# Kernel optimization log

Hardware: AMD Instinct MI355X
Metric: run time of the kernel (lower is better)

Reference implementation:

```python
import jax, jax.numpy as jnp
import numpy as np

H = 501
T = 200
V = 71


def gru_layer(x, h0, W_ih, W_hh, b_ih, b_hh):
    # x: [B,T,I], h0: [B,H]; PyTorch GRU gate order: r, z, n
    gi = jnp.einsum('bti,gi->btg', x, W_ih) + b_ih  # [B,T,3H]

    def step(h, gi_t):
        gh = h @ W_hh.T + b_hh  # [B,3H]
        r = jax.nn.sigmoid(gi_t[:, :H] + gh[:, :H])
        z = jax.nn.sigmoid(gi_t[:, H:2 * H] + gh[:, H:2 * H])
        n = jnp.tanh(gi_t[:, 2 * H:] + r * gh[:, 2 * H:])
        h_new = (1.0 - z) * n + z * h
        return h_new, h_new

    h_last, ys = jax.lax.scan(step, h0, jnp.swapaxes(gi, 0, 1))
    return jnp.swapaxes(ys, 0, 1), h_last  # [B,T,H], [B,H]


def setup_inputs() -> dict:
    key = jax.random.key(0)
    ks = jax.random.split(key, 16)
    s = 1.0 / np.sqrt(H)
    u = lambda k, shp: jax.random.uniform(k, shp, jnp.float32, -s, s)
    return {
        'x': jax.random.normal(ks[0], (256, 1), jnp.float32),
        'W_ih1': u(ks[1], (3 * H, 1)), 'W_hh1': u(ks[2], (3 * H, H)),
        'b_ih1': u(ks[3], (3 * H,)), 'b_hh1': u(ks[4], (3 * H,)),
        'W_ih2': u(ks[5], (3 * H, H)), 'W_hh2': u(ks[6], (3 * H, H)),
        'b_ih2': u(ks[7], (3 * H,)), 'b_hh2': u(ks[8], (3 * H,)),
        'W_ih3': u(ks[9], (3 * H, H)), 'W_hh3': u(ks[10], (3 * H, H)),
        'b_ih3': u(ks[11], (3 * H,)), 'b_hh3': u(ks[12], (3 * H,)),
        'Wd': u(ks[13], (V, H)), 'bd': u(ks[14], (V,)),
    }


def reference(x, W_ih1, W_hh1, b_ih1, b_hh1, W_ih2, W_hh2, b_ih2, b_hh2,
              W_ih3, W_hh3, b_ih3, b_hh3, Wd, bd):
    B = x.shape[0]
    # repeat_vector: tile latent scalar across T timesteps -> [B,T,1]
    xr = jnp.broadcast_to(x[:, None, :], (B, T, 1))
    h0 = jnp.zeros((B, H), x.dtype)
    o1, h1 = gru_layer(xr, h0, W_ih1, W_hh1, b_ih1, b_hh1)
    o1 = jnp.tanh(o1)
    o2, h2 = gru_layer(o1, h1, W_ih2, W_hh2, b_ih2, b_hh2)
    o2 = jnp.tanh(o2)
    o3, _ = gru_layer(o2, h2, W_ih3, W_hh3, b_ih3, b_hh3)
    o3 = jnp.tanh(o3)
    logits = jax.nn.relu(jnp.einsum('bth,vh->btv', o3, Wd) + bd)  # [B,T,V]
    return logits
```

## Files before the change

### kernel.cpp

```cpp
#include <hip/hip_runtime.h>
#include <hip/hip_fp16.h>

typedef _Float16 half8 __attribute__((ext_vector_type(8)));
typedef float floatx16 __attribute__((ext_vector_type(16)));

#define HID 501
#define TT  200
#define BB  256
#define VV  71
#define HP  512

#define OFF_BAR   0ull
#define OFF_HFRAG 4096ull
#define SZ_HFRAG  (2ull*8*32*512*2)
#define OFF_HFIN  (OFF_HFRAG + SZ_HFRAG)
#define SZ_HFIN   (256ull*512*4)
#define OFF_GI1   (OFF_HFIN + SZ_HFIN)
#define SZ_GI1    (256ull*1536*4)
#define OFF_BIAS  (OFF_GI1 + SZ_GI1)
#define SZ_BIAS   (65536ull)
#define OFF_WD    (OFF_BIAS + SZ_BIAS)
#define SZ_WD     (96ull*512*2)
#define OFF_BD    (OFF_WD + SZ_WD)
#define SZ_BD     4096ull
#define OFF_W     (OFF_BD + SZ_BD)
#define SZ_W      (3ull*2*32*2*32*1024*2)
#define OFF_OFRAG (OFF_W + SZ_W)
#define SZ_OBUF   (8ull*200*32*512*2)
#define WS_NEED   (OFF_OFRAG + 2ull*SZ_OBUF)

#define COH_LD16(dst, p) \
  asm volatile("global_load_dwordx4 %0, %1, off sc0 sc1" : "=&v"(dst) : "v"(p) : "memory")
__device__ __forceinline__ void coh_store16(_Float16* p, half8 v) {
  asm volatile("global_store_dwordx4 %0, %1, off sc0 sc1" :: "v"(p), "v"(v) : "memory");
}
__device__ __forceinline__ void coh_st4(unsigned* p, unsigned v) {
  asm volatile("global_store_dword %0, %1, off sc0 sc1" :: "v"(p), "v"(v) : "memory");
}
__device__ __forceinline__ float tanh_fast(float x) {
  float e = __expf(2.f*x);
  return 1.f - 2.f/(e + 1.f);
}

__global__ __launch_bounds__(256) void prep_weights(
    const float* __restrict__ wih1, const float* __restrict__ whh1,
    const float* __restrict__ wih2, const float* __restrict__ whh2,
    const float* __restrict__ wih3, const float* __restrict__ whh3,
    _Float16* __restrict__ wbuf)
{
  const float* WIH[3] = {wih1, wih2, wih3};
  const float* WHH[3] = {whh1, whh2, whh3};
  const long total = 3ll << 21;
  for (long idx = (long)blockIdx.x*256 + threadIdx.x; idx < total; idx += (long)gridDim.x*256) {
    int k   = (int)(idx & 1023);
    int row = (int)((idx >> 10) & 31);
    int rt  = (int)((idx >> 15) & 1);
    int blk = (int)((idx >> 16) & 31);
    int L   = (int)(idx >> 21);
    int g, hl; bool ok;
    if (rt == 0) { g = row >> 4; hl = row & 15; ok = true; }
    else         { g = 2;        hl = row & 15; ok = (row < 16); }
    int hcol = blk*16 + hl;
    ok = ok && (hcol < HID);
    float w = 0.f;
    if (ok) {
      if (k < HP) { if (L > 0 && k < HID) w = WIH[L][(g*HID + hcol)*HID + k]; }
      else        { int kk = k - HP; if (kk < HID) w = WHH[L][(g*HID + hcol)*HID + kk]; }
    }
    _Float16 wh = (_Float16)w;
    _Float16 wl = (_Float16)(w - (float)wh);
    long oh = ((((long)(L*2+0)*32 + blk)*2 + rt)*32 + row)*1024 + k;
    long ol = ((((long)(L*2+1)*32 + blk)*2 + rt)*32 + row)*1024 + k;
    wbuf[oh] = wh;
    wbuf[ol] = wl;
  }
}

__global__ __launch_bounds__(256) void prep_misc(
    const float* __restrict__ x, const float* __restrict__ wih1,
    const float* __restrict__ bih1, const float* __restrict__ bhh1,
    const float* __restrict__ bih2, const float* __restrict__ bhh2,
    const float* __restrict__ bih3, const float* __restrict__ bhh3,
    const float* __restrict__ wd, const float* __restrict__ bd,
    float* __restrict__ gi1, float* __restrict__ bias,
    _Float16* __restrict__ wdbuf, float* __restrict__ bdbuf)
{
  const int N1 = 256*1536;
  const int N2 = 3*2*1536;
  const int N3 = 96*512;
  const int N4 = 96;
  for (int idx = blockIdx.x*256 + threadIdx.x; idx < N1+N2+N3+N4; idx += gridDim.x*256) {
    if (idx < N1) {
      int b = idx / 1536, m = idx % 1536;
      int g = m >> 9, hc = m & 511;
      float v = 0.f;
      if (hc < HID) { int r = g*HID + hc; v = x[b]*wih1[r] + bih1[r]; }
      gi1[idx] = v;
    } else if (idx < N1+N2) {
      int i2 = idx - N1;
      int L = i2 / (2*1536);
      int rest = i2 % (2*1536);
      int pl = rest / 1536, m = rest % 1536;
      int g = m >> 9, hc = m & 511;
      float v = 0.f;
      if (hc < HID) {
        int r = g*HID + hc;
        if (pl == 0) v = (L==0) ? 0.f : (L==1 ? bih2[r] : bih3[r]);
        else         v = (L==0) ? bhh1[r] : (L==1 ? bhh2[r] : bhh3[r]);
      }
      bias[i2] = v;
    } else if (idx < N1+N2+N3) {
      int i3 = idx - (N1+N2);
      int v = i3 >> 9, k = i3 & 511;
      float val = (v < VV && k < HID) ? wd[v*HID + k] : 0.f;
      wdbuf[i3] = (_Float16)val;
    } else {
      int v = idx - (N1+N2+N3);
      bdbuf[v] = (v < VV) ? bd[v] : 0.f;
    }
  }
}

template<int L>
__global__ __launch_bounds__(512, 1) void gru_layer_k(
    const _Float16* __restrict__ wbuf,
    const _Float16* __restrict__ osrc,
    _Float16* __restrict__ odst,
    _Float16* __restrict__ hfrag,
    float* __restrict__ hfin,
    const float* __restrict__ gi1,
    const float* __restrict__ bias,
    unsigned* __restrict__ flags)
{
  constexpr int KPW = (L==0) ? 4 : 8;
  const int bid  = blockIdx.x;
  const int tile = bid & 7;
  const int sl   = bid >> 3;
  const int tid  = threadIdx.x;
  const int w    = tid >> 6;
  const int lane = tid & 63;

  __shared__ float    ldsC[8][2][32][32];
  __shared__ _Float16 ldsH[2][32][16];

  half8 Wf[2][2][KPW];
  {
    int row = lane & 31;
    int kc  = (lane >> 5) << 3;
    int ks0 = (L==0) ? (32 + w*4) : (w*8);
    #pragma unroll
    for (int pl = 0; pl < 2; ++pl)
      #pragma unroll
      for (int rt = 0; rt < 2; ++rt)
        #pragma unroll
        for (int i = 0; i < KPW; ++i) {
          long off = ((((long)(L*2+pl)*32 + sl)*2 + rt)*32 + row)*1024 + (long)(ks0+i)*16 + kc;
          Wf[pl][rt][i] = *(const half8*)(wbuf + off);
        }
  }

  const int b     = tid & 31;
  const int hl    = (tid >> 5) & 15;
  const int bglob = tile*32 + b;
  const int hglob = sl*16 + hl;
  float hreg = 0.f;
  float bih[3], bhh[3], gi[3] = {0,0,0};
  if (L > 0) hreg = hfin[bglob*HP + hglob];
  #pragma unroll
  for (int g = 0; g < 3; ++g) {
    bih[g] = bias[(L*2+0)*1536 + g*512 + hglob];
    bhh[g] = bias[(L*2+1)*1536 + g*512 + hglob];
    if (L == 0) gi[g] = gi1[(long)bglob*1536 + g*512 + hglob];
  }

  const long hf_par  = 8ll*32*512;
  const long hf_tile = (long)tile*(32*512);
  const long ob_t    = (long)tile*200*(32*512);
  const long region  = (long)sl*512;
  unsigned* fl = flags + tile*32;
  unsigned dead = 0;

  half8 X[8];
  if (L > 0 && w < 4) {
    const _Float16* xb = osrc + ob_t + (long)(w*8)*512 + lane*8;
    #pragma unroll
    for (int i = 0; i < 8; ++i) X[i] = *(const half8*)(xb + i*512);
  }

  for (int t = 0; t < TT; ++t) {
    if (L > 0 && w < 4) {
      floatx16 C0, C1;
      #pragma unroll
      for (int i = 0; i < 16; ++i) { C0[i] = 0.f; C1[i] = 0.f; }
      #pragma unroll
      for (int i = 0; i < 8; ++i) {
        C0 = __builtin_amdgcn_mfma_f32_32x32x16_f16(Wf[0][0][i], X[i], C0, 0, 0, 0);
        C0 = __builtin_amdgcn_mfma_f32_32x32x16_f16(Wf[1][0][i], X[i], C0, 0, 0, 0);
        C1 = __builtin_amdgcn_mfma_f32_32x32x16_f16(Wf[0][1][i], X[i], C1, 0, 0, 0);
        C1 = __builtin_amdgcn_mfma_f32_32x32x16_f16(Wf[1][1][i], X[i], C1, 0, 0, 0);
      }
      {
        int tn = (t + 1 < TT) ? t + 1 : 0;
        const _Float16* xb = osrc + ob_t + (long)tn*(32*512) + (long)(w*8)*512 + lane*8;
        #pragma unroll
        for (int i = 0; i < 8; ++i) X[i] = *(const half8*)(xb + i*512);
      }
      int col = lane & 31, rb = (lane >> 5) << 2;
      #pragma unroll
      for (int r = 0; r < 16; ++r) {
        int rowm = (r & 3) + 8*(r >> 2) + rb;
        ldsC[w][0][rowm][col] = C0[r];
        ldsC[w][1][rowm][col] = C1[r];
      }
    }
    if (t > 0) __syncthreads();
    if ((L == 0 || w >= 4) && !(L == 0 && t == 0)) {
      const int hs0 = (L==0) ? (w*4) : ((w-4)*8);
      const _Float16* hp = hfrag + (long)(t & 1)*hf_par + hf_tile + (long)hs0*512 + lane*8;
      half8 H[KPW];
      #pragma unroll
      for (int i = 0; i < KPW; ++i) COH_LD16(H[i], hp + i*512);
      asm volatile("s_waitcnt vmcnt(0)" ::: "memory");
      __builtin_amdgcn_sched_barrier(0);
      floatx16 C0, C1;
      #pragma unroll
      for (int i = 0; i < 16; ++i) { C0[i] = 0.f; C1[i] = 0.f; }
      #pragma unroll
      for (int i = 0; i < KPW; ++i) {
        C0 = __builtin_amdgcn_mfma_f32_32x32x16_f16(Wf[0][0][i], H[i], C0, 0, 0, 0);
        C0 = __builtin_amdgcn_mfma_f32_32x32x16_f16(Wf[1][0][i], H[i], C0, 0, 0, 0);
        C1 = __builtin_amdgcn_mfma_f32_32x32x16_f16(Wf[0][1][i], H[i], C1, 0, 0, 0);
        C1 = __builtin_amdgcn_mfma_f32_32x32x16_f16(Wf[1][1][i], H[i], C1, 0, 0, 0);
      }
      int col = lane & 31, rb = (lane >> 5) << 2;
      #pragma unroll
      for (int r = 0; r < 16; ++r) {
        int rowm = (r & 3) + 8*(r >> 2) + rb;
        ldsC[w][0][rowm][col] = C0[r];
        ldsC[w][1][rowm][col] = C1[r];
      }
    }
    __syncthreads();
    {
      float sx[3] = {0,0,0}, sh[3] = {0,0,0};
      if (!(L == 0 && t == 0)) {
        #pragma unroll
        for (int g = 0; g < 3; ++g) {
          int rt  = (g == 2) ? 1 : 0;
          int row = (g == 2) ? hl : g*16 + hl;
          float ax = 0.f, ah = 0.f;
          if (L == 0) {
            #pragma unroll
            for (int ww = 0; ww < 8; ++ww) ah += ldsC[ww][rt][row][b];
          } else {
            #pragma unroll
            for (int ww = 0; ww < 4; ++ww) ax += ldsC[ww][rt][row][b];
            #pragma unroll
            for (int ww = 4; ww < 8; ++ww) ah += ldsC[ww][rt][row][b];
          }
          sx[g] = ax; sh[g] = ah;
        }
      }
      float pr = sx[0] + gi[0] + bih[0] + sh[0] + bhh[0];
      float pz = sx[1] + gi[1] + bih[1] + sh[1] + bhh[1];
      float r = 1.f/(1.f + __expf(-pr));
      float z = 1.f/(1.f + __expf(-pz));
      float n = tanh_fast(sx[2] + gi[2] + bih[2] + r*(sh[2] + bhh[2]));
      float hn = (1.f - z)*n + z*hreg;
      hreg = hn;
      ldsH[0][b][hl] = (_Float16)hn;
      ldsH[1][b][hl] = (_Float16)tanh_fast(hn);
      if (t == TT-1) hfin[bglob*HP + hglob] = hn;
    }
    __syncthreads();
    if (tid < 64) {
      int h0 = (tid >> 5) * 8;
      half8 hv = *(const half8*)&ldsH[0][tid & 31][h0];
      coh_store16(hfrag + (long)((t+1) & 1)*hf_par + hf_tile + region + tid*8, hv);
    }
    if (w == 0) {
      asm volatile("s_waitcnt vmcnt(0)" ::: "memory");
      if (tid == 0 && t < TT-1)
        coh_st4(fl + sl, (unsigned)(L*(TT-1) + t + 1));
    }
    if (tid < 64) {
      int h0 = (tid >> 5) * 8;
      half8 ov = *(const half8*)&ldsH[1][tid & 31][h0];
      *(half8*)(odst + ob_t + (long)t*(32*512) + region + tid*8) = ov;
    }
    if (w == 5 && t < TT-1 && !dead) {
      const unsigned tgt = (unsigned)(L*(TT-1) + t + 1);
      const unsigned* fp = fl + (lane & 31);
      unsigned tries = 0;
      for (;;) {
        unsigned v0, v1, v2, v3;
        asm volatile(
          "global_load_dword %0, %4, off sc0 sc1\n\t"
          "global_load_dword %1, %4, off sc0 sc1\n\t"
          "global_load_dword %2, %4, off sc0 sc1\n\t"
          "global_load_dword %3, %4, off sc0 sc1"
          : "=&v"(v0), "=&v"(v1), "=&v"(v2), "=&v"(v3)
          : "v"(fp) : "memory");
        asm volatile("s_waitcnt vmcnt(3)" ::: "memory");
        __builtin_amdgcn_sched_barrier(0);
        if (__all(v0 >= tgt)) break;
        asm volatile("s_waitcnt vmcnt(2)" ::: "memory");
        __builtin_amdgcn_sched_barrier(0);
        if (__all(v1 >= tgt)) break;
        asm volatile("s_waitcnt vmcnt(1)" ::: "memory");
        __builtin_amdgcn_sched_barrier(0);
        if (__all(v2 >= tgt)) break;
        asm volatile("s_waitcnt vmcnt(0)" ::: "memory");
        __builtin_amdgcn_sched_barrier(0);
        if (__all(v3 >= tgt)) break;
        if (++tries > (1u<<17)) { dead = 1; break; }
      }
      asm volatile("s_waitcnt vmcnt(0)" ::: "memory");
    }
  }
}

__global__ __launch_bounds__(256, 2) void decoder_k(
    const _Float16* __restrict__ o3,
    const _Float16* __restrict__ wdbuf,
    const float* __restrict__ bdbuf,
    float* __restrict__ out)
{
  const int bx = blockIdx.x;
  const int tile = bx & 7;
  const int chunk = bx >> 3;
  const int tid = threadIdx.x;
  const int w = tid >> 6, lane = tid & 63;
  __shared__ float ldsD[4][96][32];
  __shared__ float ldsO[32][73];

  half8 Wf[3][8];
  {
    int kc = (lane >> 5) << 3;
    #pragma unroll
    for (int mt = 0; mt < 3; ++mt)
      #pragma unroll
      for (int i = 0; i < 8; ++i) {
        int row = mt*32 + (lane & 31);
        int k = (w*8 + i)*16 + kc;
        Wf[mt][i] = *(const half8*)(wdbuf + (long)row*512 + k);
      }
  }
  for (int tt = 0; tt < 8; ++tt) {
    int t = chunk*8 + tt;
    long ob = ((long)tile*200 + t)*(32*512);
    half8 Xf[8];
    #pragma unroll
    for (int i = 0; i < 8; ++i) {
      int s = w*8 + i;
      Xf[i] = *(const half8*)(o3 + ob + (long)s*512 + lane*8);
    }
    floatx16 C0, C1, C2;
    #pragma unroll
    for (int i = 0; i < 16; ++i) { C0[i] = 0.f; C1[i] = 0.f; C2[i] = 0.f; }
    #pragma unroll
    for (int i = 0; i < 8; ++i) {
      C0 = __builtin_amdgcn_mfma_f32_32x32x16_f16(Wf[0][i], Xf[i], C0, 0, 0, 0);
      C1 = __builtin_amdgcn_mfma_f32_32x32x16_f16(Wf[1][i], Xf[i], C1, 0, 0, 0);
      C2 = __builtin_amdgcn_mfma_f32_32x32x16_f16(Wf[2][i], Xf[i], C2, 0, 0, 0);
    }
    {
      int col = lane & 31;
      int rb = (lane >> 5) << 2;
      #pragma unroll
      for (int r = 0; r < 16; ++r) {
        int rowm = (r & 3) + 8*(r >> 2) + rb;
        ldsD[w][rowm][col]      = C0[r];
        ldsD[w][32 + rowm][col] = C1[r];
        ldsD[w][64 + rowm][col] = C2[r];
      }
    }
    __syncthreads();
    for (int ii = tid; ii < VV*32; ii += 256) {
      int bb = ii & 31, v = ii >> 5;
      float s = ldsD[0][v][bb] + ldsD[1][v][bb] + ldsD[2][v][bb] + ldsD[3][v][bb] + bdbuf[v];
      ldsO[bb][v] = s > 0.f ? s : 0.f;
    }
    __syncthreads();
    for (int ii = tid; ii < VV*32; ii += 256) {
      int bb = ii / VV, v = ii - bb*VV;
      out[((long)(tile*32 + bb)*200 + t)*VV + v] = ldsO[bb][v];
    }
    __syncthreads();
  }
}

extern "C" void kernel_launch(void* const* d_in, const int* in_sizes, int n_in,
                              void* d_out, int out_size, void* d_ws, size_t ws_size,
                              hipStream_t stream) {
  (void)in_sizes; (void)n_in;
  const float* x    = (const float*)d_in[0];
  const float* wih1 = (const float*)d_in[1];
  const float* whh1 = (const float*)d_in[2];
  const float* bih1 = (const float*)d_in[3];
  const float* bhh1 = (const float*)d_in[4];
  const float* wih2 = (const float*)d_in[5];
  const float* whh2 = (const float*)d_in[6];
  const float* bih2 = (const float*)d_in[7];
  const float* bhh2 = (const float*)d_in[8];
  const float* wih3 = (const float*)d_in[9];
  const float* whh3 = (const float*)d_in[10];
  const float* bih3 = (const float*)d_in[11];
  const float* bhh3 = (const float*)d_in[12];
  const float* wd   = (const float*)d_in[13];
  const float* bd   = (const float*)d_in[14];
  char* ws = (char*)d_ws;

  if (ws_size < WS_NEED) {
    hipMemsetAsync(d_out, 0, (size_t)out_size*sizeof(float), stream);
    return;
  }

  _Float16* wbuf   = (_Float16*)(ws + OFF_W);
  float*    gi1p   = (float*)(ws + OFF_GI1);
  float*    biasp  = (float*)(ws + OFF_BIAS);
  _Float16* wdbufp = (_Float16*)(ws + OFF_WD);
  float*    bdbufp = (float*)(ws + OFF_BD);
  _Float16* hfragp = (_Float16*)(ws + OFF_HFRAG);
  float*    hfinp  = (float*)(ws + OFF_HFIN);
  unsigned* flagsp = (unsigned*)(ws + OFF_BAR);
  _Float16* ob0    = (_Float16*)(ws + OFF_OFRAG);
  _Float16* ob1    = ob0 + SZ_OBUF/2;

  hipMemsetAsync(ws + OFF_BAR, 0, 4096, stream);

  prep_weights<<<4096, 256, 0, stream>>>(wih1, whh1, wih2, whh2, wih3, whh3, wbuf);
  prep_misc<<<1024, 256, 0, stream>>>(x, wih1, bih1, bhh1, bih2, bhh2, bih3, bhh3,
                                      wd, bd, gi1p, biasp, wdbufp, bdbufp);

  gru_layer_k<0><<<256, 512, 0, stream>>>(wbuf, ob1, ob0, hfragp, hfinp, gi1p, biasp, flagsp);
  gru_layer_k<1><<<256, 512, 0, stream>>>(wbuf, ob0, ob1, hfragp, hfinp, gi1p, biasp, flagsp);
  gru_layer_k<2><<<256, 512, 0, stream>>>(wbuf, ob1, ob0, hfragp, hfinp, gi1p, biasp, flagsp);

  decoder_k<<<200, 256, 0, stream>>>(ob0, wdbufp, bdbufp, (float*)d_out);
}
```

Measured before the change: 2.030 ms.

## Compute next-step input projection one timestep ahead with double-buffered LDS partials

The input-projection MFMAs for layers 2 and 3 now compute timestep t+1 during step t, with the first step computed before the loop. Partial results go into a double-buffered LDS region that the gate reduction reads by parity. The aim is to take the W_ih matmul off the per-step critical path that waits on the recurrent h exchange. In exchange LDS grows from 8 to 12 partial slots, and the X global loads now sit just before their MFMAs rather than being prefetched a step early.

After: 2.170 ms. +6.9%, slower.

```diff
diff --git a/kernel.cpp b/kernel.cpp
--- a/kernel.cpp
+++ b/kernel.cpp
@@ -140,7 +140,7 @@
   const int w    = tid >> 6;
   const int lane = tid & 63;
 
-  __shared__ float    ldsC[8][2][32][32];
+  __shared__ float    ldsP[12][2][32][32];
   __shared__ _Float16 ldsH[2][32][16];
 
   half8 Wf[2][2][KPW];
@@ -180,15 +180,36 @@
   unsigned* fl = flags + tile*32;
   unsigned dead = 0;
 
-  half8 X[8];
   if (L > 0 && w < 4) {
     const _Float16* xb = osrc + ob_t + (long)(w*8)*512 + lane*8;
+    half8 X[8];
     #pragma unroll
     for (int i = 0; i < 8; ++i) X[i] = *(const half8*)(xb + i*512);
+    floatx16 C0, C1;
+    #pragma unroll
+    for (int i = 0; i < 16; ++i) { C0[i] = 0.f; C1[i] = 0.f; }
+    #pragma unroll
+    for (int i = 0; i < 8; ++i) {
+      C0 = __builtin_amdgcn_mfma_f32_32x32x16_f16(Wf[0][0][i], X[i], C0, 0, 0, 0);
+      C0 = __builtin_amdgcn_mfma_f32_32x32x16_f16(Wf[1][0][i], X[i], C0, 0, 0, 0);
+      C1 = __builtin_amdgcn_mfma_f32_32x32x16_f16(Wf[0][1][i], X[i], C1, 0, 0, 0);
+      C1 = __builtin_amdgcn_mfma_f32_32x32x16_f16(Wf[1][1][i], X[i], C1, 0, 0, 0);
+    }
+    int col = lane & 31, rb = (lane >> 5) << 2;
+    #pragma unroll
+    for (int r = 0; r < 16; ++r) {
+      int rowm = (r & 3) + 8*(r >> 2) + rb;
+      ldsP[4 + w][0][rowm][col] = C0[r];
+      ldsP[4 + w][1][rowm][col] = C1[r];
+    }
   }
 
   for (int t = 0; t < TT; ++t) {
-    if (L > 0 && w < 4) {
+    if (L > 0 && w < 4 && t + 1 < TT) {
+      const _Float16* xb = osrc + ob_t + (long)(t+1)*(32*512) + (long)(w*8)*512 + lane*8;
+      half8 X[8];
+      #pragma unroll
+      for (int i = 0; i < 8; ++i) X[i] = *(const half8*)(xb + i*512);
       floatx16 C0, C1;
       #pragma unroll
       for (int i = 0; i < 16; ++i) { C0[i] = 0.f; C1[i] = 0.f; }
@@ -199,18 +220,13 @@
         C1 = __builtin_amdgcn_mfma_f32_32x32x16_f16(Wf[0][1][i], X[i], C1, 0, 0, 0);
         C1 = __builtin_amdgcn_mfma_f32_32x32x16_f16(Wf[1][1][i], X[i], C1, 0, 0, 0);
       }
-      {
-        int tn = (t + 1 < TT) ? t + 1 : 0;
-        const _Float16* xb = osrc + ob_t + (long)tn*(32*512) + (long)(w*8)*512 + lane*8;
-        #pragma unroll
-        for (int i = 0; i < 8; ++i) X[i] = *(const half8*)(xb + i*512);
-      }
+      int slot = 4 + (((t+1) & 1) << 2) + w;
       int col = lane & 31, rb = (lane >> 5) << 2;
       #pragma unroll
       for (int r = 0; r < 16; ++r) {
         int rowm = (r & 3) + 8*(r >> 2) + rb;
-        ldsC[w][0][rowm][col] = C0[r];
-        ldsC[w][1][rowm][col] = C1[r];
+        ldsP[slot][0][rowm][col] = C0[r];
+        ldsP[slot][1][rowm][col] = C1[r];
       }
     }
     if (t > 0) __syncthreads();
@@ -232,12 +248,13 @@
         C1 = __builtin_amdgcn_mfma_f32_32x32x16_f16(Wf[0][1][i], H[i], C1, 0, 0, 0);
         C1 = __builtin_amdgcn_mfma_f32_32x32x16_f16(Wf[1][1][i], H[i], C1, 0, 0, 0);
       }
+      int slot = (L==0) ? w : (w - 4);
       int col = lane & 31, rb = (lane >> 5) << 2;
       #pragma unroll
       for (int r = 0; r < 16; ++r) {
         int rowm = (r & 3) + 8*(r >> 2) + rb;
-        ldsC[w][0][rowm][col] = C0[r];
-        ldsC[w][1][rowm][col] = C1[r];
+        ldsP[slot][0][rowm][col] = C0[r];
+        ldsP[slot][1][rowm][col] = C1[r];
       }
     }
     __syncthreads();
@@ -251,12 +268,13 @@
           float ax = 0.f, ah = 0.f;
           if (L == 0) {
             #pragma unroll
-            for (int ww = 0; ww < 8; ++ww) ah += ldsC[ww][rt][row][b];
+            for (int ww = 0; ww < 8; ++ww) ah += ldsP[ww][rt][row][b];
           } else {
             #pragma unroll
-            for (int ww = 0; ww < 4; ++ww) ax += ldsC[ww][rt][row][b];
+            for (int ww = 0; ww < 4; ++ww) ah += ldsP[ww][rt][row][b];
+            const int xb0 = 4 + ((t & 1) << 2);
             #pragma unroll
-            for (int ww = 4; ww < 8; ++ww) ah += ldsC[ww][rt][row][b];
+            for (int ww = 0; ww < 4; ++ww) ax += ldsP[xb0 + ww][rt][row][b];
           }
           sx[g] = ax; sh[g] = ah;
         }
```
